# Optimization experiments

Measured on AMD Instinct MI355X. Metric: run time of the kernel, lower is better.

## Reference

```python
import jax, jax.numpy as jnp
import numpy as np

B, T, M, H = 256, 64, 256, 256


def setup_inputs() -> dict:
    key = jax.random.key(0)
    ks = jax.random.split(key, 16)
    n = jax.random.normal
    s = 0.05  # small init so tanh/sigmoid stay in sane range
    return {
        "enc_inputs": n(ks[0], (T, B, M), jnp.float32),  # module transposes (0,1) itself
        "y": n(ks[1], (B, T, 1), jnp.float32),
        "W_d": n(ks[2], (M, 2 * H), jnp.float32) * s,
        "b_Wd": n(ks[3], (M,), jnp.float32) * s,
        "U_d": n(ks[4], (M, M), jnp.float32) * s,
        "v_d": n(ks[5], (1, M), jnp.float32) * s,
        "w_tilda": n(ks[6], (1, M + 1), jnp.float32) * s,
        "b_wt": n(ks[7], (1,), jnp.float32) * s,
        "W_ih": n(ks[8], (4 * H, 1), jnp.float32) * s,
        "W_hh": n(ks[9], (4 * H, H), jnp.float32) * s,
        "b_ih": n(ks[10], (4 * H,), jnp.float32) * s,
        "b_hh": n(ks[11], (4 * H,), jnp.float32) * s,
        "W_y": n(ks[12], (H, H + M), jnp.float32) * s,
        "b_Wy": n(ks[13], (H,), jnp.float32) * s,
        "v_y": n(ks[14], (1, H), jnp.float32) * s,
        "b_vy": n(ks[15], (1,), jnp.float32) * s,
    }


def reference(enc_inputs, y, W_d, b_Wd, U_d, v_d, w_tilda, b_wt,
              W_ih, W_hh, b_ih, b_hh, W_y, b_Wy, v_y, b_vy):
    enc = jnp.swapaxes(enc_inputs, 0, 1)                 # (B,T,M)
    # U_d(enc) is loop-invariant; hoist (same math as recomputing per step)
    y1 = jnp.einsum('btm,nm->btn', enc, U_d)             # (B,T,M)
    ys = jnp.swapaxes(y, 0, 1)                           # (T,B,1) scanned over time
    b = enc.shape[0]
    d0 = jnp.zeros((b, H), enc.dtype)
    s0 = jnp.zeros((b, H), enc.dtype)
    c0 = jnp.zeros((b, M), enc.dtype)

    def step(carry, y_t):
        d, sp, _ = carry
        # Bahdanau-style temporal attention over encoder steps
        x1 = jnp.concatenate([d, sp], axis=1) @ W_d.T + b_Wd      # (B,M)
        l = jnp.tanh(x1[:, None, :] + y1) @ v_d[0]                # (B,T)
        beta = jax.nn.softmax(l, axis=1)
        c = jnp.einsum('bt,btm->bm', beta, enc)                   # (B,M)
        # scalar driving input for the decoder LSTM cell
        y_til = jnp.concatenate([c, y_t], axis=1) @ w_tilda.T + b_wt  # (B,1)
        # torch.nn.LSTMCell update with (h, c) = (d, sp)
        gates = y_til @ W_ih.T + b_ih + d @ W_hh.T + b_hh         # (B,4H)
        i, f, g, o = jnp.split(gates, 4, axis=1)
        sp_new = jax.nn.sigmoid(f) * sp + jax.nn.sigmoid(i) * jnp.tanh(g)
        d_new = jax.nn.sigmoid(o) * jnp.tanh(sp_new)
        return (d_new, sp_new, c), None

    (d, sp, c), _ = jax.lax.scan(step, (d0, s0, c0), ys)
    h = jnp.concatenate([d, c], axis=1) @ W_y.T + b_Wy            # (B,H)
    return h @ v_y.T + b_vy                                        # (B,1)
```

## Files before the change

### kernel.cpp

```cpp
#include <hip/hip_runtime.h>


#define Bx 256
#define Tx 64
#define Mx 256
#define Hx 256
#define NT 1024
#define XS 20

typedef unsigned int  uint;
typedef unsigned short ushort;
typedef _Float16 h2  __attribute__((ext_vector_type(2)));
typedef float    f2v __attribute__((ext_vector_type(2)));

__device__ __forceinline__ float4 ld4(const float* p) { return *(const float4*)p; }
__device__ __forceinline__ float h2f(ushort s) {
  union { ushort s; _Float16 h; } c; c.s = s; return (float)c.h;
}
__device__ __forceinline__ ushort f2h(float f) {
  union { _Float16 h; ushort s; } c; c.h = (_Float16)f; return c.s;
}
__device__ __forceinline__ uint pk2(float a, float b) {
  return (uint)f2h(a) | ((uint)f2h(b) << 16);
}

#if defined(__has_builtin)
#if __has_builtin(__builtin_amdgcn_rcpf)
#define RCPF(x) __builtin_amdgcn_rcpf(x)
#endif
#if __has_builtin(__builtin_amdgcn_fdot2)
#define HAVE_FDOT2 1
#endif
#if __has_builtin(__builtin_amdgcn_cvt_pk_f32_fp8) && __has_builtin(__builtin_amdgcn_cvt_pk_fp8_f32)
#define HAVE_FP8 1
#endif
#endif
#ifndef RCPF
#define RCPF(x) (1.0f / (x))
#endif

__device__ __forceinline__ float tanh_fast(float x) {
  float e2 = __expf(2.0f * x);
  return 1.0f - 2.0f * RCPF(e2 + 1.0f);
}
__device__ __forceinline__ float tanh_pre(float z2) {
  return 1.0f - 2.0f * RCPF(__expf(z2) + 1.0f);
}
__device__ __forceinline__ float sigm(float x) {
  return RCPF(1.0f + __expf(-x));
}
__device__ __forceinline__ float wave_sum(float v) {
  #pragma unroll
  for (int o = 1; o < 64; o <<= 1) v += __shfl_xor(v, o, 64);
  return v;
}
__device__ __forceinline__ int xsw(int m) { return (m >> 4) * XS + (m & 15); }

__device__ __forceinline__ float dot2u(uint w, uint a, float acc) {
#ifdef HAVE_FDOT2
  h2 W = __builtin_bit_cast(h2, w);
  h2 A = __builtin_bit_cast(h2, a);
  return __builtin_amdgcn_fdot2(W, A, acc, false);
#else
  return acc + h2f((ushort)w) * h2f((ushort)a)
             + h2f((ushort)(w >> 16)) * h2f((ushort)(a >> 16));
#endif
}

__device__ __forceinline__ uint sw8(float f) {
  union { float f; uint u; } c; c.f = f;
  uint s = (c.u >> 31) << 7;
  float a = fabsf(f);
  if (!(a >= 0.0009765625f)) return s;
  if (a >= 448.f) return s | 0x7e;
  int e = (int)((c.u >> 23) & 0xff) - 127;
  if (e < -6) { int q = (int)(a * 512.f + 0.5f); return s | (uint)q; }
  uint m = ((c.u & 0x7fffff) + 0x80000) >> 20;
  if (m == 8) { m = 0; ++e; }
  if (e > 8) return s | 0x7e;
  return s | ((uint)(e + 7) << 3) | m;
}
__device__ __forceinline__ float sw8d(uint b) {
  uint s = b >> 7, e = (b >> 3) & 0xf, m = b & 7;
  float v;
  if (e) { union { uint u; float f; } c; c.u = ((e + 120u) << 23) | (m << 20); v = c.f; }
  else v = (float)m * 0.001953125f;
  return s ? -v : v;
}
__device__ __forceinline__ uint pk_fp8x4(float w0, float w1, float w2, float w3) {
#ifdef HAVE_FP8
  int u = 0;
  u = __builtin_amdgcn_cvt_pk_fp8_f32(w0, w1, u, false);
  u = __builtin_amdgcn_cvt_pk_fp8_f32(w2, w3, u, true);
  return (uint)u;
#else
  return sw8(w0) | (sw8(w1) << 8) | (sw8(w2) << 16) | (sw8(w3) << 24);
#endif
}
template <bool HI>
__device__ __forceinline__ f2v dec2(uint w) {
#ifdef HAVE_FP8
  return __builtin_amdgcn_cvt_pk_f32_fp8((int)w, HI);
#else
  uint b0 = HI ? ((w >> 16) & 0xffu) : (w & 0xffu);
  uint b1 = HI ? (w >> 24) : ((w >> 8) & 0xffu);
  return f2v{sw8d(b0), sw8d(b1)};
#endif
}
__device__ __forceinline__ f2v dotq(uint w, float4 a, f2v acc) {
  acc += dec2<false>(w) * f2v{a.x, a.y};
  acc += dec2<true>(w)  * f2v{a.z, a.w};
  return acc;
}

__global__ __launch_bounds__(256)
void pack_weights(const float* __restrict__ W_d,
                  const float* __restrict__ W_hh,
                  const float* __restrict__ U_d,
                  const float* __restrict__ W_y,
                  uint4* __restrict__ WhhH,
                  uint4* __restrict__ Wd8q,
                  uint4* __restrict__ Ud8,
                  float* __restrict__ Wyt) {
  const int blk = blockIdx.x, tid = threadIdx.x;
  if (blk < 32) {
    const int c = blk;
    #pragma unroll
    for (int q = 0; q < 4; ++q) {
      const int j = tid + 256 * q;
      const float* wr = W_hh + (size_t)j * 256 + 8 * c;
      float4 a = ld4(wr), b = ld4(wr + 4);
      WhhH[c * 1024 + j] = uint4{pk2(a.x, a.y), pk2(a.z, a.w),
                                 pk2(b.x, b.y), pk2(b.z, b.w)};
    }
  } else if (blk < 64) {
    const int k16 = blk - 32;
    const float* wr = W_d + (size_t)tid * 512 + 16 * k16;
    float4 a = ld4(wr), b = ld4(wr + 4), c = ld4(wr + 8), d = ld4(wr + 12);
    uint4 u;
    u.x = pk_fp8x4(16.f * a.x, 16.f * a.y, 16.f * a.z, 16.f * a.w);
    u.y = pk_fp8x4(16.f * b.x, 16.f * b.y, 16.f * b.z, 16.f * b.w);
    u.z = pk_fp8x4(16.f * c.x, 16.f * c.y, 16.f * c.z, 16.f * c.w);
    u.w = pk_fp8x4(16.f * d.x, 16.f * d.y, 16.f * d.z, 16.f * d.w);
    Wd8q[k16 * 256 + tid] = u;
  } else if (blk < 96) {
    const int m8 = blk - 64;
    float4 a = ld4(U_d + (size_t)tid * 256 + 8 * m8);
    float4 b = ld4(U_d + (size_t)tid * 256 + 8 * m8 + 4);
    Ud8[m8 * 256 + tid] = uint4{pk2(2.f * a.x, 2.f * a.y), pk2(2.f * a.z, 2.f * a.w),
                                pk2(2.f * b.x, 2.f * b.y), pk2(2.f * b.z, 2.f * b.w)};
  } else {
    const int k0 = (blk - 96) * 4;
    float4 w = ld4(W_y + (size_t)tid * 512 + k0);
    Wyt[(k0 + 0) * 256 + tid] = w.x;
    Wyt[(k0 + 1) * 256 + tid] = w.y;
    Wyt[(k0 + 2) * 256 + tid] = w.z;
    Wyt[(k0 + 3) * 256 + tid] = w.w;
  }
}

__global__ __launch_bounds__(NT, 1)
void fused(const float* __restrict__ enc,
           const float* __restrict__ yv,
           const float* __restrict__ b_Wd,
           const float* __restrict__ v_d,
           const float* __restrict__ w_tilda,
           const float* __restrict__ b_wt,
           const float* __restrict__ W_ih,
           const float* __restrict__ b_ih,
           const float* __restrict__ b_hh,
           const float* __restrict__ b_Wy,
           const float* __restrict__ v_y,
           const float* __restrict__ b_vy,
           const uint4* __restrict__ WhhH,
           const uint4* __restrict__ Wd8q,
           const uint4* __restrict__ Ud8,
           const float* __restrict__ Wyt,
           ushort* __restrict__ Y1,
           float* __restrict__ out)
{
  extern __shared__ __align__(16) uint4 wdl[];
  __shared__ __align__(16) float dsp_s[2 * Hx];
  __shared__ __align__(16) ushort dsph_s[Hx];
  __shared__ __align__(16) float xq_s[2 * 16 * XS];
  __shared__ __align__(16) float vd_s[16 * XS];
  __shared__ float gates_s[1024];
  __shared__ float dcfin_s[2 * Hx];
  __shared__ float l_s[Tx];
  __shared__ uint  beta2_s[Tx / 2];
  __shared__ float e_s[Tx];
  __shared__ float red_s[4];
  __shared__ float ytil_s;
  __shared__ unsigned flagX, flagL, flagE;

  const int b   = blockIdx.x;
  const int tid = threadIdx.x;
  const int h   = tid & 255;
  const int p   = tid >> 8;
  const size_t BM = (size_t)Bx * Mx;

  #pragma unroll
  for (int i = 0; i < 8; ++i) wdl[i * NT + tid] = Wd8q[i * NT + tid];
  if (tid < 256) vd_s[xsw(tid)] = v_d[tid];
  if (tid < 512) dsp_s[tid] = 0.0f;
  if (tid < 256) dsph_s[tid] = 0;
  if (tid == 0) { flagX = 0u; flagL = 0u; flagE = 0u; }

  float bj0 = 0.f, bj1 = 0.f;
  if (tid < 512) { bj0 = b_ih[tid] + b_hh[tid]; bj1 = b_ih[tid + 512] + b_hh[tid + 512]; }
  float bWd_r = 0.f;
  if (tid >= 512 && tid < 768) bWd_r = 2.0f * b_Wd[tid - 512];
  float wih0 = 0.f, wih1 = 0.f, wih2 = 0.f, wih3 = 0.f;
  if (tid < 256) {
    wih0 = W_ih[tid]; wih1 = W_ih[tid + 256]; wih2 = W_ih[tid + 512]; wih3 = W_ih[tid + 768];
  }
  float yv_r = 0.f;
  if (tid >= 512 && tid < 576) yv_r = yv[b * Tx + (tid - 512)];
  const float wty = w_tilda[Mx];
  const float bwt = b_wt[0];

  if (tid < Tx) {
    const float* er = enc + (size_t)tid * BM + (size_t)b * Mx;
    float acc = 0.0f;
    for (int m = 0; m < Mx; m += 4) {
      float4 e4 = ld4(er + m);
      float4 w4 = ld4(w_tilda + m);
      acc += e4.x * w4.x + e4.y * w4.y + e4.z * w4.z + e4.w * w4.w;
    }
    e_s[tid] = acc;
  }

  {
    const int n = h;
    const float* eb = enc + (size_t)b * Mx;
    for (int tb = p * 16; tb < p * 16 + 16; tb += 8) {
      f2v acc2[8];
      #pragma unroll
      for (int j = 0; j < 8; ++j) acc2[j] = f2v{0.f, 0.f};
      #pragma unroll 2
      for (int m8 = 0; m8 < 32; ++m8) {
        uint4 u = Ud8[m8 * 256 + n];
        f2v w01 = f2v{h2f((ushort)u.x), h2f((ushort)(u.x >> 16))};
        f2v w23 = f2v{h2f((ushort)u.y), h2f((ushort)(u.y >> 16))};
        f2v w45 = f2v{h2f((ushort)u.z), h2f((ushort)(u.z >> 16))};
        f2v w67 = f2v{h2f((ushort)u.w), h2f((ushort)(u.w >> 16))};
        #pragma unroll
        for (int j = 0; j < 8; ++j) {
          const float* ep = eb + (size_t)(tb + j) * BM + 8 * m8;
          float4 ea = ld4(ep), eb4 = ld4(ep + 4);
          acc2[j] += f2v{ea.x, ea.y} * w01;
          acc2[j] += f2v{ea.z, ea.w} * w23;
          acc2[j] += f2v{eb4.x, eb4.y} * w45;
          acc2[j] += f2v{eb4.z, eb4.w} * w67;
        }
      }
      #pragma unroll
      for (int j = 0; j < 8; ++j)
        Y1[((size_t)b * Tx + tb + j) * Mx + n] = f2h(acc2[j].x + acc2[j].y);
    }
  }
  __syncthreads();

  float e_r = 0.0f;
  if (tid >= 512 && tid < 576) e_r = e_s[tid - 512];

  float sp_reg = 0.0f;

  for (int t = 0; t < Tx; ++t) {
    float gi = 0.0f, gg = 0.0f;
    if (tid < 512) {
      float ga0 = 0.f, ga1 = 0.f, gb0 = 0.f, gb1 = 0.f;
      const uint4* wp  = WhhH + tid;
      const uint4* adp = (const uint4*)dsph_s;
      #pragma unroll 2
      for (int c = 0; c < 32; ++c) {
        uint4 wa = wp[c * 1024];
        uint4 wb = wp[c * 1024 + 512];
        uint4 a  = adp[c];
        ga0 = dot2u(wa.x, a.x, ga0); ga1 = dot2u(wa.y, a.y, ga1);
        ga0 = dot2u(wa.z, a.z, ga0); ga1 = dot2u(wa.w, a.w, ga1);
        gb0 = dot2u(wb.x, a.x, gb0); gb1 = dot2u(wb.y, a.y, gb1);
        gb0 = dot2u(wb.z, a.z, gb0); gb1 = dot2u(wb.w, a.w, gb1);
      }
      gi = ga0 + ga1 + bj0;
      gg = gb0 + gb1 + bj1;
      if (tid >= 256) {
        gates_s[tid]       = gi;
        gates_s[tid + 512] = gg;
        __threadfence_block();
        if ((tid & 63) == 0)
          __hip_atomic_fetch_add(&flagE, 1u, __ATOMIC_RELEASE, __HIP_MEMORY_SCOPE_WORKGROUP);
      }
    } else {
      const int idx = tid - 512;
      const int m = idx & 255, q = idx >> 8;
      const int tq = idx >> 3, lq = idx & 7;
      const ushort* y1r = Y1 + ((size_t)b * Tx + tq) * Mx + lq * 32;
      uint4 yq0 = *(const uint4*)(y1r);
      uint4 yq1 = *(const uint4*)(y1r + 8);
      uint4 yq2 = *(const uint4*)(y1r + 16);
      uint4 yq3 = *(const uint4*)(y1r + 24);
      {
        f2v xa2 = f2v{0.f, 0.f};
        const uint4* xp = wdl + m + (q * 16) * 256;
        #pragma unroll 4
        for (int i = 0; i < 16; ++i) {
          uint4 u = xp[i * 256];
          const float4* ap = (const float4*)dsp_s + 64 * q + 4 * i;
          float4 a0 = ap[0], a1 = ap[1], a2 = ap[2], a3 = ap[3];
          xa2 = dotq(u.x, a0, xa2); xa2 = dotq(u.y, a1, xa2);
          xa2 = dotq(u.z, a2, xa2); xa2 = dotq(u.w, a3, xa2);
        }
        xq_s[q * (16 * XS) + xsw(m)] = (xa2.x + xa2.y) * 0.125f
                                     + (q == 0 ? bWd_r : 0.0f);
      }
      __threadfence_block();
      if ((threadIdx.x & 63) == 0)
        __hip_atomic_fetch_add(&flagX, 1u, __ATOMIC_RELEASE, __HIP_MEMORY_SCOPE_WORKGROUP);
      const unsigned tgtX = 8u * (unsigned)(t + 1);
      while (__hip_atomic_load(&flagX, __ATOMIC_ACQUIRE, __HIP_MEMORY_SCOPE_WORKGROUP) < tgtX) {}

      {
        float ps = 0.0f;
        uint yy[8] = {yq0.x, yq0.y, yq0.z, yq0.w, yq1.x, yq1.y, yq1.z, yq1.w};
        uint zz[8] = {yq2.x, yq2.y, yq2.z, yq2.w, yq3.x, yq3.y, yq3.z, yq3.w};
        #pragma unroll
        for (int g = 0; g < 8; ++g) {
          const int c   = 2 * lq + (g >> 2);
          const int off = c * XS + 4 * (g & 3);
          float4 xa0 = *(const float4*)(xq_s + off);
          float4 xa1 = *(const float4*)(xq_s + 16 * XS + off);
          float4 vv  = *(const float4*)(vd_s + off);
          uint ya = (g < 4) ? yy[2 * g] : zz[2 * (g - 4)];
          uint yb = (g < 4) ? yy[2 * g + 1] : zz[2 * (g - 4) + 1];
          ps += tanh_pre(xa0.x + xa1.x + h2f((ushort)ya)) * vv.x
              + tanh_pre(xa0.y + xa1.y + h2f((ushort)(ya >> 16))) * vv.y
              + tanh_pre(xa0.z + xa1.z + h2f((ushort)yb)) * vv.z
              + tanh_pre(xa0.w + xa1.w + h2f((ushort)(yb >> 16))) * vv.w;
        }
        ps += __shfl_xor(ps, 1, 64);
        ps += __shfl_xor(ps, 2, 64);
        ps += __shfl_xor(ps, 4, 64);
        if (lq == 0) l_s[tq] = ps;
      }
      __threadfence_block();
      if ((threadIdx.x & 63) == 0)
        __hip_atomic_fetch_add(&flagL, 1u, __ATOMIC_RELEASE, __HIP_MEMORY_SCOPE_WORKGROUP);

      if (idx < 64) {
        __builtin_amdgcn_s_setprio(1);
        const unsigned tgtL = 8u * (unsigned)(t + 1);
        while (__hip_atomic_load(&flagL, __ATOMIC_ACQUIRE, __HIP_MEMORY_SCOPE_WORKGROUP) < tgtL) {}
        float e0  = __expf(l_s[idx]);
        float den = e0;
        float num = e0 * e_r;
        #pragma unroll
        for (int o = 1; o < 64; o <<= 1) {
          den += __shfl_xor(den, o, 64);
          num += __shfl_xor(num, o, 64);
        }
        if (t == Tx - 1) {
          float beta = e0 * RCPF(den);
          float bn = __shfl_xor(beta, 1, 64);
          if (!(idx & 1)) beta2_s[idx >> 1] = pk2(beta, bn);
        }
        if (idx == t) ytil_s = num * RCPF(den) + wty * yv_r + bwt;
        __threadfence_block();
        if (idx == 0)
          __hip_atomic_fetch_add(&flagE, 1u, __ATOMIC_RELEASE, __HIP_MEMORY_SCOPE_WORKGROUP);
        __builtin_amdgcn_s_setprio(0);
      }
    }

    if (tid < 256) {
      const unsigned tgtE = 5u * (unsigned)(t + 1);
      while (__hip_atomic_load(&flagE, __ATOMIC_ACQUIRE, __HIP_MEMORY_SCOPE_WORKGROUP) < tgtE) {}
      __builtin_amdgcn_s_setprio(1);
      const float ytil = ytil_s;
      float fi = sigm(gi                  + ytil * wih0);
      float ff = sigm(gates_s[256 + tid]  + ytil * wih1);
      float fg = tanh_fast(gg             + ytil * wih2);
      float fo = sigm(gates_s[768 + tid]  + ytil * wih3);
      float spn = ff * sp_reg + fi * fg;
      float dn  = fo * tanh_fast(spn);
      sp_reg = spn;
      dsp_s[tid]       = dn;
      dsp_s[256 + tid] = spn;
      dsph_s[tid]      = f2h(dn);
      if (t == Tx - 1) dcfin_s[tid] = dn;
      __builtin_amdgcn_s_setprio(0);
    }
    __syncthreads();
  }

  if (tid >= 512) {
    const int idx = tid - 512;
    const int m = idx >> 1, q = idx & 1;
    float acc = 0.0f;
    #pragma unroll 4
    for (int j = 0; j < 32; ++j) {
      const int tt = q * 32 + j;
      uint bp = beta2_s[tt >> 1];
      float bb = (tt & 1) ? h2f((ushort)(bp >> 16)) : h2f((ushort)bp);
      acc += bb * enc[(size_t)tt * BM + (size_t)b * Mx + m];
    }
    acc += __shfl_xor(acc, 1, 64);
    if (q == 0) dcfin_s[256 + m] = acc;
  }
  __syncthreads();

  {
    float a = 0.0f;
    const float* wy = Wyt + h;
    for (int k = 128 * p; k < 128 * p + 128; ++k)
      a += wy[(size_t)k * 256] * dcfin_s[k];
    gates_s[p * 256 + h] = a;
  }
  __syncthreads();
  if (tid < 256) {
    float aa = gates_s[h] + gates_s[256 + h] + gates_s[512 + h] + gates_s[768 + h]
             + b_Wy[h];
    float po = aa * v_y[h];
    po = wave_sum(po);
    if ((tid & 63) == 0) red_s[tid >> 6] = po;
  }
  __syncthreads();
  if (tid == 0) out[b] = red_s[0] + red_s[1] + red_s[2] + red_s[3] + b_vy[0];
}

extern "C" void kernel_launch(void* const* d_in, const int* in_sizes, int n_in,
                              void* d_out, int out_size, void* d_ws, size_t ws_size,
                              hipStream_t stream) {
  const float* enc     = (const float*)d_in[0];
  const float* yv      = (const float*)d_in[1];
  const float* W_d     = (const float*)d_in[2];
  const float* b_Wd    = (const float*)d_in[3];
  const float* U_d     = (const float*)d_in[4];
  const float* v_d     = (const float*)d_in[5];
  const float* w_tilda = (const float*)d_in[6];
  const float* b_wt    = (const float*)d_in[7];
  const float* W_ih    = (const float*)d_in[8];
  const float* W_hh    = (const float*)d_in[9];
  const float* b_ih    = (const float*)d_in[10];
  const float* b_hh    = (const float*)d_in[11];
  const float* W_y     = (const float*)d_in[12];
  const float* b_Wy    = (const float*)d_in[13];
  const float* v_y     = (const float*)d_in[14];
  const float* b_vy    = (const float*)d_in[15];
  float* outp = (float*)d_out;

  char* ws = (char*)d_ws;
  uint4* WhhH  = (uint4*)ws;
  uint4* Wd8q  = (uint4*)(ws + (512 << 10));
  uint4* Ud8   = (uint4*)(ws + (640 << 10));
  float* Wyt   = (float*)(ws + (768 << 10));
  ushort* Y1   = (ushort*)(ws + (1280 << 10));

  const int DYN_LDS = 128 << 10;
  hipFuncSetAttribute((const void*)fused,
                      hipFuncAttributeMaxDynamicSharedMemorySize, DYN_LDS);

  hipLaunchKernelGGL(pack_weights, dim3(224), dim3(256), 0, stream,
                     W_d, W_hh, U_d, W_y, WhhH, Wd8q, Ud8, Wyt);
  hipLaunchKernelGGL(fused, dim3(Bx), dim3(NT), DYN_LDS, stream,
                     enc, yv, b_Wd, v_d, w_tilda, b_wt, W_ih, b_ih, b_hh,
                     b_Wy, v_y, b_vy, WhhH, Wd8q, Ud8, Wyt, Y1, outp);
}
```

Measured before the change: 575.0 us.

## Split attention query projection across all 1024 threads in four K-quarters

The W_d·[d,sp] query projection is now computed by all four 256-thread groups, each covering a quarter of the reduction, instead of only the 512 attention threads covering halves. The LSTM gate threads take on this extra projection work before their W_hh matvec, and the attention threads then sum four partials per element. This shortens the serial per-step attention critical path. The cost is a longer path for the gate threads and larger shared-memory partial buffers.

```diff
diff --git a/kernel.cpp b/kernel.cpp
--- a/kernel.cpp
+++ b/kernel.cpp
@@ -182,7 +182,7 @@
   extern __shared__ __align__(16) uint4 wdl[];
   __shared__ __align__(16) float dsp_s[2 * Hx];
   __shared__ __align__(16) ushort dsph_s[Hx];
-  __shared__ __align__(16) float xq_s[2 * 16 * XS];
+  __shared__ __align__(16) float xq_s[4 * 16 * XS];
   __shared__ __align__(16) float vd_s[16 * XS];
   __shared__ float gates_s[1024];
   __shared__ float dcfin_s[2 * Hx];
@@ -197,6 +197,8 @@
   const int tid = threadIdx.x;
   const int h   = tid & 255;
   const int p   = tid >> 8;
+  const int mq  = tid & 255;
+  const int qq  = tid >> 8;
   const size_t BM = (size_t)Bx * Mx;
 
   #pragma unroll
@@ -209,7 +211,7 @@
   float bj0 = 0.f, bj1 = 0.f;
   if (tid < 512) { bj0 = b_ih[tid] + b_hh[tid]; bj1 = b_ih[tid + 512] + b_hh[tid + 512]; }
   float bWd_r = 0.f;
-  if (tid >= 512 && tid < 768) bWd_r = 2.0f * b_Wd[tid - 512];
+  if (tid < 256) bWd_r = 2.0f * b_Wd[tid];
   float wih0 = 0.f, wih1 = 0.f, wih2 = 0.f, wih3 = 0.f;
   if (tid < 256) {
     wih0 = W_ih[tid]; wih1 = W_ih[tid + 256]; wih2 = W_ih[tid + 512]; wih3 = W_ih[tid + 768];
@@ -267,6 +269,35 @@
   float sp_reg = 0.0f;
 
   for (int t = 0; t < Tx; ++t) {
+    uint4 yq0, yq1, yq2, yq3;
+    if (tid >= 512) {
+      const int idx = tid - 512;
+      const int tq = idx >> 3, lq = idx & 7;
+      const ushort* y1r = Y1 + ((size_t)b * Tx + tq) * Mx + lq * 32;
+      yq0 = *(const uint4*)(y1r);
+      yq1 = *(const uint4*)(y1r + 8);
+      yq2 = *(const uint4*)(y1r + 16);
+      yq3 = *(const uint4*)(y1r + 24);
+    }
+
+    {
+      f2v xa2 = f2v{0.f, 0.f};
+      const uint4* xp = wdl + mq + (qq * 8) * 256;
+      #pragma unroll
+      for (int i = 0; i < 8; ++i) {
+        uint4 u = xp[i * 256];
+        const float4* ap = (const float4*)dsp_s + 4 * (qq * 8 + i);
+        float4 a0 = ap[0], a1 = ap[1], a2 = ap[2], a3 = ap[3];
+        xa2 = dotq(u.x, a0, xa2); xa2 = dotq(u.y, a1, xa2);
+        xa2 = dotq(u.z, a2, xa2); xa2 = dotq(u.w, a3, xa2);
+      }
+      xq_s[qq * (16 * XS) + xsw(mq)] = (xa2.x + xa2.y) * 0.125f
+                                     + (qq == 0 ? bWd_r : 0.0f);
+    }
+    __threadfence_block();
+    if ((tid & 63) == 0)
+      __hip_atomic_fetch_add(&flagX, 1u, __ATOMIC_RELEASE, __HIP_MEMORY_SCOPE_WORKGROUP);
+
     float gi = 0.0f, gg = 0.0f;
     if (tid < 512) {
       float ga0 = 0.f, ga1 = 0.f, gb0 = 0.f, gb1 = 0.f;
@@ -293,31 +324,8 @@
       }
     } else {
       const int idx = tid - 512;
-      const int m = idx & 255, q = idx >> 8;
       const int tq = idx >> 3, lq = idx & 7;
-      const ushort* y1r = Y1 + ((size_t)b * Tx + tq) * Mx + lq * 32;
-      uint4 yq0 = *(const uint4*)(y1r);
-      uint4 yq1 = *(const uint4*)(y1r + 8);
-      uint4 yq2 = *(const uint4*)(y1r + 16);
-      uint4 yq3 = *(const uint4*)(y1r + 24);
-      {
-        f2v xa2 = f2v{0.f, 0.f};
-        const uint4* xp = wdl + m + (q * 16) * 256;
-        #pragma unroll 4
-        for (int i = 0; i < 16; ++i) {
-          uint4 u = xp[i * 256];
-          const float4* ap = (const float4*)dsp_s + 64 * q + 4 * i;
-          float4 a0 = ap[0], a1 = ap[1], a2 = ap[2], a3 = ap[3];
-          xa2 = dotq(u.x, a0, xa2); xa2 = dotq(u.y, a1, xa2);
-          xa2 = dotq(u.z, a2, xa2); xa2 = dotq(u.w, a3, xa2);
-        }
-        xq_s[q * (16 * XS) + xsw(m)] = (xa2.x + xa2.y) * 0.125f
-                                     + (q == 0 ? bWd_r : 0.0f);
-      }
-      __threadfence_block();
-      if ((threadIdx.x & 63) == 0)
-        __hip_atomic_fetch_add(&flagX, 1u, __ATOMIC_RELEASE, __HIP_MEMORY_SCOPE_WORKGROUP);
-      const unsigned tgtX = 8u * (unsigned)(t + 1);
+      const unsigned tgtX = 16u * (unsigned)(t + 1);
       while (__hip_atomic_load(&flagX, __ATOMIC_ACQUIRE, __HIP_MEMORY_SCOPE_WORKGROUP) < tgtX) {}
 
       {
@@ -328,15 +336,17 @@
         for (int g = 0; g < 8; ++g) {
           const int c   = 2 * lq + (g >> 2);
           const int off = c * XS + 4 * (g & 3);
-          float4 xa0 = *(const float4*)(xq_s + off);
-          float4 xa1 = *(const float4*)(xq_s + 16 * XS + off);
-          float4 vv  = *(const float4*)(vd_s + off);
+          float4 x0 = *(const float4*)(xq_s + off);
+          float4 x1 = *(const float4*)(xq_s + 320 + off);
+          float4 x2 = *(const float4*)(xq_s + 640 + off);
+          float4 x3 = *(const float4*)(xq_s + 960 + off);
+          float4 vv = *(const float4*)(vd_s + off);
           uint ya = (g < 4) ? yy[2 * g] : zz[2 * (g - 4)];
           uint yb = (g < 4) ? yy[2 * g + 1] : zz[2 * (g - 4) + 1];
-          ps += tanh_pre(xa0.x + xa1.x + h2f((ushort)ya)) * vv.x
-              + tanh_pre(xa0.y + xa1.y + h2f((ushort)(ya >> 16))) * vv.y
-              + tanh_pre(xa0.z + xa1.z + h2f((ushort)yb)) * vv.z
-              + tanh_pre(xa0.w + xa1.w + h2f((ushort)(yb >> 16))) * vv.w;
+          ps += tanh_pre(x0.x + x1.x + x2.x + x3.x + h2f((ushort)ya)) * vv.x
+              + tanh_pre(x0.y + x1.y + x2.y + x3.y + h2f((ushort)(ya >> 16))) * vv.y
+              + tanh_pre(x0.z + x1.z + x2.z + x3.z + h2f((ushort)yb)) * vv.z
+              + tanh_pre(x0.w + x1.w + x2.w + x3.w + h2f((ushort)(yb >> 16))) * vv.w;
         }
         ps += __shfl_xor(ps, 1, 64);
         ps += __shfl_xor(ps, 2, 64);
@@ -344,7 +354,7 @@
         if (lq == 0) l_s[tq] = ps;
       }
       __threadfence_block();
-      if ((threadIdx.x & 63) == 0)
+      if ((tid & 63) == 0)
         __hip_atomic_fetch_add(&flagL, 1u, __ATOMIC_RELEASE, __HIP_MEMORY_SCOPE_WORKGROUP);
 
       if (idx < 64) {
```

After: 583.1 us, median of 2. Within noise of the previous version (+1.4%).
